# Kernel tuning notes

Hardware: AMD Instinct MI355X
Metric: run time of the kernel (lower is better)

The kernel has to match this reference:

```python
import math
import jax, jax.numpy as jnp
import numpy as np

D = 128
B = 8
PIXEL_SIZE = 1.5
GRID_DIST = 6.0
GRID_STEP = 3.0
TOP_K = 1
MAX_SHIFT_FRACTION = 0.25


def _euler_zyz_to_matrix(ang):
    # R = Z(a) @ Y(b) @ Z(c)  (pytorch3d 'ZYZ' convention, used by RELION)
    a, b, c = ang[..., 0], ang[..., 1], ang[..., 2]
    ca, sa = jnp.cos(a), jnp.sin(a)
    cb, sb = jnp.cos(b), jnp.sin(b)
    cc, sc = jnp.cos(c), jnp.sin(c)
    one = jnp.ones_like(a)
    r0 = jnp.stack([ca * cb * cc - sa * sc, -ca * cb * sc - sa * cc, ca * sb], -1)
    r1 = jnp.stack([sa * cb * cc + ca * sc, -sa * cb * sc + ca * cc, sa * sb], -1)
    r2 = jnp.stack([-sb * cc, sb * sc, cb * one], -1)
    return jnp.stack([r0, r1, r2], -2)


def _matrix_to_euler_zyz(R):
    b = jnp.arccos(jnp.clip(R[..., 2, 2], -1.0, 1.0))
    a = jnp.arctan2(R[..., 1, 2], R[..., 0, 2])
    c = jnp.arctan2(R[..., 2, 1], -R[..., 2, 0])
    return jnp.stack([a, b, c], -1)


def _so3_delta_grid():
    n = math.ceil(GRID_DIST * 2 / GRID_STEP)
    n = n if n % 2 == 1 else n + 1
    v = jnp.linspace(-GRID_DIST, GRID_DIST, n, dtype=jnp.float32)
    return jnp.stack(jnp.meshgrid(v, v, v, indexing='ij'), -1).reshape(-1, 3)


def _circular_mask(d):
    r = d // 2
    c = d // 2
    yy, xx = jnp.meshgrid(jnp.arange(d) - c, jnp.arange(d) - c, indexing='ij')
    return (yy * yy + xx * xx <= r * r).astype(jnp.float32)


def _fft_volume(vol):
    # fftshifted rfft of the (centered) volume, as in compute_dft
    d = jnp.fft.fftshift(vol, axes=(-3, -2, -1))
    d = jnp.fft.rfftn(d, axes=(-3, -2, -1))
    return jnp.fft.fftshift(d, axes=(-3, -2))


def _fft_images(imgs):
    d = jnp.fft.fftshift(imgs, axes=(-2, -1))
    d = jnp.fft.rfftn(d, axes=(-2, -1))
    return jnp.fft.fftshift(d, axes=(-2,))


def _trilinear_complex(vol, coords):
    # vol: (D, D, D//2+1) complex; coords: (..., 3) float zyx array indices.
    # Zero-padding outside the volume (grid_sample-like).
    shp = jnp.array(vol.shape, jnp.int32)
    c0f = jnp.floor(coords)
    frac = coords - c0f
    c0 = c0f.astype(jnp.int32)
    out = jnp.zeros(coords.shape[:-1], dtype=vol.dtype)
    for dz in (0, 1):
        for dy in (0, 1):
            for dx in (0, 1):
                sel = jnp.array([dz, dy, dx], bool)
                ci = c0 + jnp.array([dz, dy, dx], jnp.int32)
                w = jnp.where(sel, frac, 1.0 - frac).prod(-1)
                valid = jnp.all((ci >= 0) & (ci < shp), axis=-1)
                cc = jnp.clip(ci, 0, shp - 1)
                v = vol[cc[..., 0], cc[..., 1], cc[..., 2]]
                out = out + jnp.where(valid, w, 0.0) * v
    return out


def _extract_central_slices_rfft(vol_rfft, rotmats):
    # rotmats rotate xyz coords; volume dft is fftshifted along (-3,-2).
    d = vol_rfft.shape[0]
    fy = jnp.fft.fftshift(jnp.fft.fftfreq(d)).astype(jnp.float32)
    fx = jnp.fft.rfftfreq(d).astype(jnp.float32)
    gy, gx = jnp.meshgrid(fy, fx, indexing='ij')
    grid = jnp.stack([jnp.zeros_like(gy), gy, gx], -1)  # (d, d//2+1, 3) zyx, z=0 plane
    Rz = rotmats[..., ::-1, ::-1]  # xyz matrix -> acts on zyx coords
    coords = jnp.einsum('nij,hwj->nhwi', Rz, grid)  # (n, h, w, 3)
    conj_mask = coords[..., 2] < 0  # redundant half -> conjugate symmetry
    coords = jnp.where(conj_mask[..., None], -coords, coords)
    idx = jnp.stack([coords[..., 0] * d + d // 2,
                     coords[..., 1] * d + d // 2,
                     coords[..., 2] * d], -1)
    samples = _trilinear_complex(vol_rfft, idx)
    return jnp.where(conj_mask, jnp.conj(samples), samples)


def _forward(vol, imgs, ctfs, rotmats):
    d = vol.shape[-1]
    bsize = imgs.shape[0]
    imgs = imgs * _circular_mask(d)
    fparts = _fft_images(imgs)  # (B, d, d//2+1)
    vol_rfft = _fft_volume(vol)
    euler_degs = jnp.rad2deg(_matrix_to_euler_zyz(rotmats))  # (B, 3)
    delta = _so3_delta_grid()  # (O, 3)
    n_opts = delta.shape[0]
    expanded = delta[None] + euler_degs[:, None]  # (B, O, 3)
    rot = _euler_zyz_to_matrix(jnp.deg2rad(expanded.reshape(-1, 3)))
    projs = _extract_central_slices_rfft(vol_rfft, rot)
    projs = projs.reshape(bsize, n_opts, d, d // 2 + 1)
    projs = projs * ctfs[:, None].astype(projs.dtype)  # CTF multiply
    # FFT cross-correlation
    prod = fparts[:, None] * jnp.conj(projs)
    prod = jnp.fft.ifftshift(prod, axes=(-2,))
    corrs = jnp.fft.fftshift(jnp.fft.irfftn(prod, s=(d, d), axes=(-2, -1)), axes=(-2, -1))
    # constrained peak search within max_shift_fraction window around zero shift
    ctr = d // 2
    hw = int(MAX_SHIFT_FRACTION * d)
    win = corrs[..., ctr - hw:ctr + hw, ctr - hw:ctr + hw]
    flat = win.reshape(bsize, n_opts, -1)
    amax = jnp.argmax(flat, axis=-1)
    maxcorr = jnp.take_along_axis(flat, amax[..., None], -1)[..., 0]  # (B, O)
    row = amax // (2 * hw) + (ctr - hw)
    col = amax % (2 * hw) + (ctr - hw)
    shifts_xy = jnp.stack([col, row], -1)  # (B, O, 2) in full-image pixel coords
    # top-k over rotation candidates
    top_v, top_i = jax.lax.top_k(maxcorr, TOP_K)
    sel_shifts = jnp.take_along_axis(shifts_xy, top_i[..., None], axis=1)
    sel_euler = jnp.take_along_axis(expanded, top_i[..., None], axis=1)
    mean = maxcorr.mean(-1, keepdims=True)
    std = jnp.std(maxcorr, axis=-1, ddof=1, keepdims=True)
    weight = 0.5 * (1.0 + jax.lax.erf((top_v - mean) / ((std + 1e-6) * jnp.sqrt(jnp.float32(2.0)))))
    pred_shifts_angs = -(sel_shifts.astype(jnp.float32) - 0.5 * d) * PIXEL_SIZE
    pred_rotmats = _euler_zyz_to_matrix(jnp.deg2rad(sel_euler))
    return top_v, pred_rotmats, pred_shifts_angs, weight


def setup_inputs():
    key = jax.random.key(0)
    k1, k2, k3, k4 = jax.random.split(key, 4)
    vol = jax.random.normal(k1, (D, D, D), jnp.float32)
    imgs = jax.random.normal(k2, (B, D, D), jnp.float32)
    ctfs = jax.random.uniform(k3, (B, D, D // 2 + 1), jnp.float32, -1.0, 1.0)
    ang = jax.random.uniform(k4, (B, 3), jnp.float32, 0.2, 2.8)
    rotmats = _euler_zyz_to_matrix(ang)
    return {"vol": vol, "imgs": imgs, "ctfs": ctfs, "rotmats": rotmats}


def reference(vol, imgs, ctfs, rotmats):
    return _forward(vol, imgs, ctfs, rotmats)
```

## Files before the change

### kernel.cpp

```cpp
#include <hip/hip_runtime.h>
#include <hip/hip_fp16.h>
#include <math.h>

#define DIMN 128
#define KXN  65
#define NBATCH 8
#define NOPT 125

__device__ __forceinline__ void fft_twiddles(float sigma, int lane,
                                             float* twr, float* twi){
  const float W = 0.04908738521234052f;
  float s, c;
  sincosf(sigma * W * (float)lane, &s, &c);
  twr[0] = c; twi[0] = s;
#pragma unroll
  for (int st = 1; st <= 6; ++st){
    int off = 64 >> st;
    int m = (lane & (off - 1)) << st;
    sincosf(sigma * W * (float)m, &s, &c);
    bool hi = (lane & off) != 0;
    twr[st] = hi ? c : 1.f;
    twi[st] = hi ? s : 0.f;
  }
}

__device__ __forceinline__ void wave_fft128(float& Ar, float& Ai, float& Br, float& Bi,
                                            const float* twr, const float* twi, int lane){
  {
    float dr = Ar - Br, di = Ai - Bi;
    Ar += Br; Ai += Bi;
    float nr = dr*twr[0] - di*twi[0];
    Bi = dr*twi[0] + di*twr[0];
    Br = nr;
  }
#pragma unroll
  for (int s = 1; s <= 6; ++s){
    int off = 64 >> s;
    float sgn = (lane & off) ? -1.f : 1.f;
    float pr = __shfl_xor(Ar, off, 64);
    float pi = __shfl_xor(Ai, off, 64);
    float dr = fmaf(Ar, sgn, pr);
    float di = fmaf(Ai, sgn, pi);
    Ar = dr*twr[s] - di*twi[s];
    Ai = dr*twi[s] + di*twr[s];
    pr = __shfl_xor(Br, off, 64);
    pi = __shfl_xor(Bi, off, 64);
    dr = fmaf(Br, sgn, pr);
    di = fmaf(Bi, sgn, pi);
    Br = dr*twr[s] - di*twi[s];
    Bi = dr*twi[s] + di*twr[s];
  }
}

__device__ __forceinline__ int bitrev7(int lane){
  return (int)(__brev((unsigned)lane) >> 25);
}

__device__ __forceinline__ float2 h2f2(unsigned u){
  union { unsigned u; __half2 h; } cv; cv.u = u;
  return __half22float2(cv.h);
}
__device__ __forceinline__ unsigned f2h2(float re, float im){
  union { unsigned u; __half2 h; } cv;
  cv.h = __float22half2_rn(make_float2(re, im));
  return cv.u;
}

__global__ __launch_bounds__(256) void k_pre1(const float* __restrict__ vol,
                                              const float* __restrict__ imgs,
                                              const float* __restrict__ ctfs,
                                              const float* __restrict__ rotm,
                                              float2* __restrict__ A_T,
                                              float2* __restrict__ AI_T,
                                              float* __restrict__ cfT,
                                              float* __restrict__ mats){
  __shared__ float2 Zbuf[4][128];
  __shared__ float Xr[65][9];
  __shared__ float Xi[65][9];
  int bid = blockIdx.x;
  int t = threadIdx.x, lane = t & 63, w = t >> 6;

  if (bid < 2176){
    bool isimg = (bid >= 2048);
    const float* src = isimg ? imgs : vol;
    float2* dst = isimg ? AI_T : A_T;
    int l0 = (isimg ? (bid - 2048) : bid) * 8;
    int l1 = l0 + 2*w, l2 = l1 + 1;
    float m1a = 1.f, m1b = 1.f, m2a = 1.f, m2b = 1.f;
    if (isimg){
      int y1 = l1 & 127, y2 = y1 + 1;
      int dy1 = y1 - 64, dy2 = y2 - 64;
      int dxa = lane - 64, dxb = lane;
      m1a = (dy1*dy1 + dxa*dxa <= 4096) ? 1.f : 0.f;
      m1b = (dy1*dy1 + dxb*dxb <= 4096) ? 1.f : 0.f;
      m2a = (dy2*dy2 + dxa*dxa <= 4096) ? 1.f : 0.f;
      m2b = (dy2*dy2 + dxb*dxb <= 4096) ? 1.f : 0.f;
    }
    float twr[7], twi[7];
    fft_twiddles(-1.f, lane, twr, twi);
    float Ar = src[l1*DIMN + lane]*m1a,      Ai = src[l2*DIMN + lane]*m2a;
    float Br = src[l1*DIMN + lane + 64]*m1b, Bi = src[l2*DIMN + lane + 64]*m2b;
    wave_fft128(Ar, Ai, Br, Bi, twr, twi, lane);
    int e = bitrev7(lane);
    Zbuf[w][e]   = make_float2(Ar, Ai);
    Zbuf[w][e+1] = make_float2(Br, Bi);
    __syncthreads();
    {
      int k = lane, m = (128 - k) & 127;
      float2 zk = Zbuf[w][k], zm = Zbuf[w][m];
      float s = (k & 1) ? -0.5f : 0.5f;
      int ly1 = 2*w, ly2 = ly1 + 1;
      Xr[k][ly1] = s*(zk.x + zm.x);  Xi[k][ly1] = s*(zk.y - zm.y);
      Xr[k][ly2] = s*(zk.y + zm.y);  Xi[k][ly2] = s*(zm.x - zk.x);
      if (lane == 0){
        float2 z64 = Zbuf[w][64];
        Xr[64][ly1] = z64.x; Xi[64][ly1] = 0.f;
        Xr[64][ly2] = z64.y; Xi[64][ly2] = 0.f;
      }
    }
    __syncthreads();
    int slab = l0 >> 7, y0 = l0 & 127;
    int kk = t >> 2, yo = (t & 3) * 2;
    float4 v = make_float4(Xr[kk][yo], Xi[kk][yo], Xr[kk][yo+1], Xi[kk][yo+1]);
    *(float4*)(dst + (size_t)(slab*KXN + kk)*DIMN + y0 + yo) = v;
    if (t < 4){
      int yo2 = t*2;
      float4 v2 = make_float4(Xr[64][yo2], Xi[64][yo2], Xr[64][yo2+1], Xi[64][yo2+1]);
      *(float4*)(dst + (size_t)(slab*KXN + 64)*DIMN + y0 + yo2) = v2;
    }
  } else if (bid < 2436){
    int idx = (bid - 2176)*256 + t;
    int x = idx % 65; int by = idx / 65; int y = by & 127; int b = by >> 7;
    cfT[((size_t)b*KXN + x)*DIMN + y] = ctfs[idx];
  } else {
    int tid = (bid - 2436)*256 + t;
    if (tid < NBATCH*NOPT){
      int b = tid / NOPT, o = tid - b*NOPT;
      const float* R = rotm + b*9;
      float beta  = acosf(fminf(1.f, fmaxf(-1.f, R[8])));
      float alpha = atan2f(R[5], R[2]);
      float gamma = atan2f(R[7], -R[6]);
      const float DEG = 57.29577951308232f;
      float e0 = alpha*DEG + 3.0f*(float)(o/25      - 2);
      float e1 = beta *DEG + 3.0f*(float)((o/5) % 5 - 2);
      float e2 = gamma*DEG + 3.0f*(float)(o % 5     - 2);
      const float RAD = 0.017453292519943295f;
      float sa, ca, sb, cb, sc, cc;
      sincosf(e0*RAD, &sa, &ca);
      sincosf(e1*RAD, &sb, &cb);
      sincosf(e2*RAD, &sc, &cc);
      float* m = mats + tid*12;
      m[0] = sb*sc;
      m[1] = -sa*cb*sc + ca*cc;
      m[2] = -ca*cb*sc - sa*cc;
      m[3] = -sb*cc;
      m[4] = sa*cb*cc + ca*sc;
      m[5] = ca*cb*cc - sa*sc;
      m[6] = e0; m[7] = e1; m[8] = e2;
    }
  }
}

__global__ __launch_bounds__(512) void k_pre2(const float2* __restrict__ A_T,
                                              const float2* __restrict__ AI_T,
                                              float2* __restrict__ B_T,
                                              float2* __restrict__ fpT){
  __shared__ float As[64][9], Ai_[64][9], Bs[64][9], Bi_[64][9];
  int bid = blockIdx.x;
  int t = threadIdx.x, lane = t & 63, w = t >> 6;
  float twr[7], twi[7];
  fft_twiddles(-1.f, lane, twr, twi);

  if (bid < 1040){
    int k = bid >> 4, z0 = (bid & 15) * 8;
    int col = (z0 + w)*KXN + k;
    const float2* base = A_T + (size_t)col*DIMN;
    float2 A = base[lane], B = base[lane + 64];
    wave_fft128(A.x, A.y, B.x, B.y, twr, twi, lane);
    int p = bitrev7(lane) >> 1;
    As[p][w] = A.x; Ai_[p][w] = A.y; Bs[p][w] = B.x; Bi_[p][w] = B.y;
    __syncthreads();
    int q = t >> 2, zo = (t & 3) * 2;
    int p2 = (((q & 126) + 64) & 127) >> 1;
    float4 v;
    if (q & 1) v = make_float4(-Bs[p2][zo], -Bi_[p2][zo], -Bs[p2][zo+1], -Bi_[p2][zo+1]);
    else       v = make_float4( As[p2][zo],  Ai_[p2][zo],  As[p2][zo+1],  Ai_[p2][zo+1]);
    *(float4*)(B_T + (size_t)(q*KXN + k)*DIMN + z0 + zo) = v;
  } else {
    int c0 = (bid - 1040) * 8;
    int col = c0 + w;
    const float2* base = AI_T + (size_t)col*DIMN;
    float2 A = base[lane], B = base[lane + 64];
    wave_fft128(A.x, A.y, B.x, B.y, twr, twi, lane);
    int p = bitrev7(lane) >> 1;
    As[p][w] = A.x; Ai_[p][w] = A.y; Bs[p][w] = B.x; Bi_[p][w] = B.y;
    __syncthreads();
    int c = t >> 6, qo = (t & 63) * 2;
    int p2 = ((qo + 64) & 127) >> 1;
    float4 v = make_float4(As[p2][c], Ai_[p2][c], -Bs[p2][c], -Bi_[p2][c]);
    *(float4*)(fpT + (size_t)(c0 + c)*DIMN + qo) = v;
  }
}

__global__ __launch_bounds__(512) void k_fz(const float2* __restrict__ B_T,
                                            float2* __restrict__ volF){
  __shared__ float As[64][9], Ai_[64][9], Bs[64][9], Bi_[64][9];
  int bid = blockIdx.x;
  int j = bid / 9, grp = bid - j*9;
  int k0 = grp * 8;
  int vw = (grp == 8) ? 1 : 8;
  int t = threadIdx.x, lane = t & 63, w = t >> 6;
  if (w < vw){
    float twr[7], twi[7];
    fft_twiddles(-1.f, lane, twr, twi);
    int col = j*KXN + k0 + w;
    const float2* base = B_T + (size_t)col*DIMN;
    float2 A = base[lane], B = base[lane + 64];
    wave_fft128(A.x, A.y, B.x, B.y, twr, twi, lane);
    int p = bitrev7(lane) >> 1;
    As[p][w] = A.x; Ai_[p][w] = A.y; Bs[p][w] = B.x; Bi_[p][w] = B.y;
  }
  __syncthreads();
  int q = t >> 2, ko = (t & 3) * 2;
  int p2 = (((q & 126) + 64) & 127) >> 1;
  float2* obase = volF + (size_t)(q*DIMN + j)*KXN + k0;
  if (q & 1){
    if (ko < vw)     obase[ko]   = make_float2(-Bs[p2][ko],   -Bi_[p2][ko]);
    if (ko + 1 < vw) obase[ko+1] = make_float2(-Bs[p2][ko+1], -Bi_[p2][ko+1]);
  } else {
    if (ko < vw)     obase[ko]   = make_float2( As[p2][ko],    Ai_[p2][ko]);
    if (ko + 1 < vw) obase[ko+1] = make_float2( As[p2][ko+1],  Ai_[p2][ko+1]);
  }
}

__global__ __launch_bounds__(256) void k_fat(const float2* __restrict__ volF,
                                             unsigned* __restrict__ FATh){
  int idx = blockIdx.x*256 + threadIdx.x;
  int x = idx % 65; int zy = idx / 65; int y = zy & 127; int z = zy >> 7;
  int z1 = min(z+1,127), y1 = min(y+1,127), x1 = min(x+1,64);
  const size_t s00 = ((size_t)z *128 + y )*65;
  const size_t s01 = ((size_t)z *128 + y1)*65;
  const size_t s10 = ((size_t)z1*128 + y )*65;
  const size_t s11 = ((size_t)z1*128 + y1)*65;
  float2 a0 = volF[s00+x], a1 = volF[s00+x1];
  float2 b0 = volF[s01+x], b1 = volF[s01+x1];
  float2 c0 = volF[s10+x], c1 = volF[s10+x1];
  float2 d0 = volF[s11+x], d1 = volF[s11+x1];
  uint4* o = (uint4*)(FATh + ((size_t)idx << 3));
  o[0] = make_uint4(f2h2(a0.x,a0.y), f2h2(a1.x,a1.y), f2h2(b0.x,b0.y), f2h2(b1.x,b1.y));
  o[1] = make_uint4(f2h2(c0.x,c0.y), f2h2(c1.x,c1.y), f2h2(d0.x,d0.y), f2h2(d1.x,d1.y));
}

__device__ __forceinline__ float2 prod_elem(int h, int kx,
                                            float c1z, float c1y, float c1x,
                                            float c2z, float c2y, float c2x,
                                            const unsigned* __restrict__ FATh,
                                            const float2* __restrict__ fpc,
                                            const float*  __restrict__ cfc){
  float fyv = (float)(h - 64) * 0.0078125f;
  float fxv = (float)kx * 0.0078125f;
  float cz = fyv*c1z + fxv*c2z;
  float cy = fyv*c1y + fxv*c2y;
  float cx = fyv*c1x + fxv*c2x;
  bool cj = (cx < 0.f);
  if (cj){ cz = -cz; cy = -cy; cx = -cx; }
  float pz = cz*128.f + 64.f;
  float py = cy*128.f + 64.f;
  float px = cx*128.f;
  float fz = floorf(pz), fy = floorf(py), fx = floorf(px);
  int iz = (int)fz, iy = (int)fy, ix = (int)fx;
  float tz = pz - fz, ty = py - fy, tx = px - fx;
  float wz0 = ((unsigned)iz < 128u) ? 1.f - tz : ((iz == -1) ? tz : 0.f);
  float wz1 = ((unsigned)iz < 127u) ? tz : 0.f;
  float wy0 = ((unsigned)iy < 128u) ? 1.f - ty : ((iy == -1) ? ty : 0.f);
  float wy1 = ((unsigned)iy < 127u) ? ty : 0.f;
  float wx0 = ((unsigned)ix < 65u)  ? 1.f - tx : ((ix == -1) ? tx : 0.f);
  float wx1 = ((unsigned)ix < 64u)  ? tx : 0.f;
  int bz = min(max(iz, 0), 127), by = min(max(iy, 0), 127), bx = min(max(ix, 0), 64);
  const uint4* F = (const uint4*)(FATh + ((((size_t)bz*128 + by)*65 + bx) << 3));
  uint4 u0 = F[0], u1 = F[1];
  float2 v000 = h2f2(u0.x), v001 = h2f2(u0.y), v010 = h2f2(u0.z), v011 = h2f2(u0.w);
  float2 v100 = h2f2(u1.x), v101 = h2f2(u1.y), v110 = h2f2(u1.z), v111 = h2f2(u1.w);
  float w00 = wz0*wy0, w01 = wz0*wy1, w10 = wz1*wy0, w11 = wz1*wy1;
  float ar = w00*(wx0*v000.x + wx1*v001.x) + w01*(wx0*v010.x + wx1*v011.x)
           + w10*(wx0*v100.x + wx1*v101.x) + w11*(wx0*v110.x + wx1*v111.x);
  float ai = w00*(wx0*v000.y + wx1*v001.y) + w01*(wx0*v010.y + wx1*v011.y)
           + w10*(wx0*v100.y + wx1*v101.y) + w11*(wx0*v110.y + wx1*v111.y);
  if (cj) ai = -ai;
  float ct = cfc[h];
  float Pr = ar*ct, Pi = ai*ct;
  float2 f = fpc[h];
  return make_float2(f.x*Pr + f.y*Pi, f.y*Pr - f.x*Pi);
}

__global__ __launch_bounds__(512, 8) void k_main(const unsigned* __restrict__ FATh,
                                                 const float2* __restrict__ fpT,
                                                 const float* __restrict__ cfT,
                                                 const float* __restrict__ mats,
                                                 float* __restrict__ bestv,
                                                 int* __restrict__ besti){
  __shared__ float2 Q[64*65];
  __shared__ float rvw[8];
  __shared__ int   riw[8];

  int t = threadIdx.x, lane = t & 63, g = t >> 6;
  int blk = blockIdx.x;
  int b = blk & 7;
  int o = blk >> 3;

  float twr[7], twi[7];
  fft_twiddles(1.f, lane, twr, twi);

  const float* mp = mats + (size_t)(b*NOPT + o)*12;
  float c1z = mp[0], c1y = mp[1], c1x = mp[2];
  float c2z = mp[3], c2y = mp[4], c2x = mp[5];
  const float2* fp = fpT + (size_t)b*KXN*DIMN;
  const float*  cf = cfT + (size_t)b*KXN*DIMN;

  int e = bitrev7(lane);
  int slA = (e + 32) & 127;
  bool inwin = (slA < 64);
  const float NRM = 6.103515625e-05f;

#pragma unroll 1
  for (int ci = 0; ci < 8; ++ci){
    int kx = 8*ci + g;
    const float2* fpc = fp + (size_t)kx*DIMN;
    const float*  cfc = cf + (size_t)kx*DIMN;
    float2 A = prod_elem(lane,      kx, c1z,c1y,c1x, c2z,c2y,c2x, FATh, fpc, cfc);
    float2 B = prod_elem(lane + 64, kx, c1z,c1y,c1x, c2z,c2y,c2x, FATh, fpc, cfc);
    wave_fft128(A.x, A.y, B.x, B.y, twr, twi, lane);
    if (inwin){
      Q[slA*KXN + kx]     = make_float2( A.x*NRM,  A.y*NRM);
      Q[(slA+1)*KXN + kx] = make_float2(-B.x*NRM, -B.y*NRM);
    }
  }
  if (g == 0){
    const int kx = 64;
    const float2* fpc = fp + (size_t)kx*DIMN;
    const float*  cfc = cf + (size_t)kx*DIMN;
    float2 A = prod_elem(lane,      kx, c1z,c1y,c1x, c2z,c2y,c2x, FATh, fpc, cfc);
    float2 B = prod_elem(lane + 64, kx, c1z,c1y,c1x, c2z,c2y,c2x, FATh, fpc, cfc);
    wave_fft128(A.x, A.y, B.x, B.y, twr, twi, lane);
    if (inwin){
      Q[slA*KXN + kx]     = make_float2( A.x*NRM,  A.y*NRM);
      Q[(slA+1)*KXN + kx] = make_float2(-B.x*NRM, -B.y*NRM);
    }
  }
  __syncthreads();

  float bv = -INFINITY; int bi = 0;
  int ra = 64 - lane;
#pragma unroll 1
  for (int pi = 0; pi < 4; ++pi){
    int r1 = (4*g + pi) << 1;
    float2 a1 = Q[r1*KXN + lane];
    float2 a2 = Q[(r1+1)*KXN + lane];
    float2 b1 = Q[r1*KXN + ra];
    float2 b2 = Q[(r1+1)*KXN + ra];
    if (lane == 0){ a1.y = 0.f; a2.y = 0.f; b1.y = 0.f; b2.y = 0.f; }
    else { b1.y = -b1.y; b2.y = -b2.y; }
    float zAr = a1.x - a2.y, zAi = a1.y + a2.x;
    float zBr = b1.x - b2.y, zBi = b1.y + b2.x;
    wave_fft128(zAr, zAi, zBr, zBi, twr, twi, lane);
    if (inwin){
      int i0 = (r1 << 6) + slA;
      if (zAr > bv || (zAr == bv && i0      < bi)){ bv = zAr; bi = i0; }
      if (zAi > bv || (zAi == bv && i0+64   < bi)){ bv = zAi; bi = i0+64; }
      if (zBr > bv || (zBr == bv && i0+1    < bi)){ bv = zBr; bi = i0+1; }
      if (zBi > bv || (zBi == bv && i0+65   < bi)){ bv = zBi; bi = i0+65; }
    }
  }

#pragma unroll
  for (int off = 32; off > 0; off >>= 1){
    float v2 = __shfl_down(bv, off, 64);
    int   i2 = __shfl_down(bi, off, 64);
    if (v2 > bv || (v2 == bv && i2 < bi)){ bv = v2; bi = i2; }
  }
  if (lane == 0){ rvw[g] = bv; riw[g] = bi; }
  __syncthreads();
  if (t == 0){
    float fv = rvw[0]; int fi = riw[0];
#pragma unroll
    for (int wv = 1; wv < 8; ++wv){
      float v2 = rvw[wv]; int i2 = riw[wv];
      if (v2 > fv || (v2 == fv && i2 < fi)){ fv = v2; fi = i2; }
    }
    bestv[b*NOPT + o] = fv; besti[b*NOPT + o] = fi;
  }
}

__global__ __launch_bounds__(64) void k_out(const float* __restrict__ bestv,
                                            const int* __restrict__ besti,
                                            const float* __restrict__ mats,
                                            float* __restrict__ out){
  int b = blockIdx.x;
  if (threadIdx.x != 0) return;
  float bv = -INFINITY; int bo = 0;
  for (int o = 0; o < NOPT; ++o){
    float v = bestv[b*NOPT + o];
    if (v > bv){ bv = v; bo = o; }
  }
  float sum = 0.f;
  for (int o = 0; o < NOPT; ++o) sum += bestv[b*NOPT + o];
  float mean = sum * (1.0f/125.0f);
  float ss = 0.f;
  for (int o = 0; o < NOPT; ++o){
    float d = bestv[b*NOPT + o] - mean;
    ss += d*d;
  }
  float stdv = sqrtf(ss * (1.0f/124.0f));

  int wi = besti[b*NOPT + bo];
  int row = (wi >> 6) + 32;
  int col = (wi & 63) + 32;

  out[b] = bv;
  const float* mm = mats + (size_t)(b*NOPT + bo)*12;
  const float RAD = 0.017453292519943295f;
  float sa, ca, sb, cb, sc, cc;
  sincosf(mm[6]*RAD, &sa, &ca);
  sincosf(mm[7]*RAD, &sb, &cb);
  sincosf(mm[8]*RAD, &sc, &cc);
  float* R = out + 8 + b*9;
  R[0] = ca*cb*cc - sa*sc;  R[1] = -ca*cb*sc - sa*cc;  R[2] = ca*sb;
  R[3] = sa*cb*cc + ca*sc;  R[4] = -sa*cb*sc + ca*cc;  R[5] = sa*sb;
  R[6] = -sb*cc;            R[7] = sb*sc;              R[8] = cb;
  out[80 + b*2 + 0] = -((float)col - 64.f) * 1.5f;
  out[80 + b*2 + 1] = -((float)row - 64.f) * 1.5f;
  float z = (bv - mean) / ((stdv + 1e-6f) * 1.4142135623730951f);
  out[96 + b] = 0.5f*(1.f + erff(z));
}

extern "C" void kernel_launch(void* const* d_in, const int* in_sizes, int n_in,
                              void* d_out, int out_size, void* d_ws, size_t ws_size,
                              hipStream_t stream){
  (void)in_sizes; (void)n_in; (void)out_size; (void)ws_size;
  const float* vol  = (const float*)d_in[0];
  const float* imgs = (const float*)d_in[1];
  const float* ctfs = (const float*)d_in[2];
  const float* rotm = (const float*)d_in[3];
  float* out = (float*)d_out;

  unsigned* FATh = (unsigned*)d_ws;
  float2* bufA  = (float2*)(FATh + ((size_t)DIMN*DIMN*KXN*8));
  float2* bufB  = bufA + (size_t)DIMN*DIMN*KXN;
  float2* imgT  = bufB + (size_t)DIMN*DIMN*KXN;
  float2* fpT   = imgT + (size_t)NBATCH*KXN*DIMN;
  float*  cfT   = (float*)(fpT + (size_t)NBATCH*KXN*DIMN);
  float*  mats  = cfT + (size_t)NBATCH*KXN*DIMN;
  float*  bestv = mats + 12000;
  int*    besti = (int*)(bestv + 1000);

  k_pre1<<<2440, 256, 0, stream>>>(vol, imgs, ctfs, rotm, bufA, imgT, cfT, mats);
  k_pre2<<<1105, 512, 0, stream>>>(bufA, imgT, bufB, fpT);
  k_fz<<<1152, 512, 0, stream>>>(bufB, bufA);
  k_fat<<<(DIMN*DIMN*KXN)/256, 256, 0, stream>>>(bufA, FATh);
  k_main<<<NBATCH*NOPT, 512, 0, stream>>>(FATh, fpT, cfT, mats, bestv, besti);
  k_out<<<NBATCH, 64, 0, stream>>>(bestv, besti, mats, out);
}
```

Measured before the change: 114.8 us.

## Halve fat-voxel gather table to 4-neighbour fp16 records; parallelize final reduction

The precomputed trilinear table now stores only the four z/y neighbours per voxel (16 bytes) instead of all eight corners (32 bytes). The sampler fetches two adjacent records along x to rebuild the eight corners. This halves the table-build write traffic and the workspace footprint, at the cost of two separate 16-byte loads per sample, which may coalesce worse. The main loop is also unrolled by 2, and the per-batch output reduction switches from one serial thread to a wave-level shuffle reduction.

```diff
diff --git a/kernel.cpp b/kernel.cpp
--- a/kernel.cpp
+++ b/kernel.cpp
@@ -234,27 +234,21 @@
 }
 
 __global__ __launch_bounds__(256) void k_fat(const float2* __restrict__ volF,
-                                             unsigned* __restrict__ FATh){
+                                             uint4* __restrict__ FATy){
   int idx = blockIdx.x*256 + threadIdx.x;
   int x = idx % 65; int zy = idx / 65; int y = zy & 127; int z = zy >> 7;
-  int z1 = min(z+1,127), y1 = min(y+1,127), x1 = min(x+1,64);
-  const size_t s00 = ((size_t)z *128 + y )*65;
-  const size_t s01 = ((size_t)z *128 + y1)*65;
-  const size_t s10 = ((size_t)z1*128 + y )*65;
-  const size_t s11 = ((size_t)z1*128 + y1)*65;
-  float2 a0 = volF[s00+x], a1 = volF[s00+x1];
-  float2 b0 = volF[s01+x], b1 = volF[s01+x1];
-  float2 c0 = volF[s10+x], c1 = volF[s10+x1];
-  float2 d0 = volF[s11+x], d1 = volF[s11+x1];
-  uint4* o = (uint4*)(FATh + ((size_t)idx << 3));
-  o[0] = make_uint4(f2h2(a0.x,a0.y), f2h2(a1.x,a1.y), f2h2(b0.x,b0.y), f2h2(b1.x,b1.y));
-  o[1] = make_uint4(f2h2(c0.x,c0.y), f2h2(c1.x,c1.y), f2h2(d0.x,d0.y), f2h2(d1.x,d1.y));
+  int z1 = min(z+1,127), y1 = min(y+1,127);
+  float2 a = volF[((size_t)z *128 + y )*65 + x];
+  float2 b = volF[((size_t)z *128 + y1)*65 + x];
+  float2 c = volF[((size_t)z1*128 + y )*65 + x];
+  float2 d = volF[((size_t)z1*128 + y1)*65 + x];
+  FATy[idx] = make_uint4(f2h2(a.x,a.y), f2h2(b.x,b.y), f2h2(c.x,c.y), f2h2(d.x,d.y));
 }
 
 __device__ __forceinline__ float2 prod_elem(int h, int kx,
                                             float c1z, float c1y, float c1x,
                                             float c2z, float c2y, float c2x,
-                                            const unsigned* __restrict__ FATh,
+                                            const uint4* __restrict__ FATy,
                                             const float2* __restrict__ fpc,
                                             const float*  __restrict__ cfc){
   float fyv = (float)(h - 64) * 0.0078125f;
@@ -277,10 +271,11 @@
   float wx0 = ((unsigned)ix < 65u)  ? 1.f - tx : ((ix == -1) ? tx : 0.f);
   float wx1 = ((unsigned)ix < 64u)  ? tx : 0.f;
   int bz = min(max(iz, 0), 127), by = min(max(iy, 0), 127), bx = min(max(ix, 0), 64);
-  const uint4* F = (const uint4*)(FATh + ((((size_t)bz*128 + by)*65 + bx) << 3));
-  uint4 u0 = F[0], u1 = F[1];
-  float2 v000 = h2f2(u0.x), v001 = h2f2(u0.y), v010 = h2f2(u0.z), v011 = h2f2(u0.w);
-  float2 v100 = h2f2(u1.x), v101 = h2f2(u1.y), v110 = h2f2(u1.z), v111 = h2f2(u1.w);
+  int bx1 = min(bx + 1, 64);
+  const uint4* Fb = FATy + ((size_t)bz*128 + by)*65;
+  uint4 F0 = Fb[bx], F1 = Fb[bx1];
+  float2 v000 = h2f2(F0.x), v010 = h2f2(F0.y), v100 = h2f2(F0.z), v110 = h2f2(F0.w);
+  float2 v001 = h2f2(F1.x), v011 = h2f2(F1.y), v101 = h2f2(F1.z), v111 = h2f2(F1.w);
   float w00 = wz0*wy0, w01 = wz0*wy1, w10 = wz1*wy0, w11 = wz1*wy1;
   float ar = w00*(wx0*v000.x + wx1*v001.x) + w01*(wx0*v010.x + wx1*v011.x)
            + w10*(wx0*v100.x + wx1*v101.x) + w11*(wx0*v110.x + wx1*v111.x);
@@ -293,7 +288,7 @@
   return make_float2(f.x*Pr + f.y*Pi, f.y*Pr - f.x*Pi);
 }
 
-__global__ __launch_bounds__(512, 8) void k_main(const unsigned* __restrict__ FATh,
+__global__ __launch_bounds__(512, 8) void k_main(const uint4* __restrict__ FATy,
                                                  const float2* __restrict__ fpT,
                                                  const float* __restrict__ cfT,
                                                  const float* __restrict__ mats,
@@ -322,13 +317,13 @@
   bool inwin = (slA < 64);
   const float NRM = 6.103515625e-05f;
 
-#pragma unroll 1
+#pragma unroll 2
   for (int ci = 0; ci < 8; ++ci){
     int kx = 8*ci + g;
     const float2* fpc = fp + (size_t)kx*DIMN;
     const float*  cfc = cf + (size_t)kx*DIMN;
-    float2 A = prod_elem(lane,      kx, c1z,c1y,c1x, c2z,c2y,c2x, FATh, fpc, cfc);
-    float2 B = prod_elem(lane + 64, kx, c1z,c1y,c1x, c2z,c2y,c2x, FATh, fpc, cfc);
+    float2 A = prod_elem(lane,      kx, c1z,c1y,c1x, c2z,c2y,c2x, FATy, fpc, cfc);
+    float2 B = prod_elem(lane + 64, kx, c1z,c1y,c1x, c2z,c2y,c2x, FATy, fpc, cfc);
     wave_fft128(A.x, A.y, B.x, B.y, twr, twi, lane);
     if (inwin){
       Q[slA*KXN + kx]     = make_float2( A.x*NRM,  A.y*NRM);
@@ -339,8 +334,8 @@
     const int kx = 64;
     const float2* fpc = fp + (size_t)kx*DIMN;
     const float*  cfc = cf + (size_t)kx*DIMN;
-    float2 A = prod_elem(lane,      kx, c1z,c1y,c1x, c2z,c2y,c2x, FATh, fpc, cfc);
-    float2 B = prod_elem(lane + 64, kx, c1z,c1y,c1x, c2z,c2y,c2x, FATh, fpc, cfc);
+    float2 A = prod_elem(lane,      kx, c1z,c1y,c1x, c2z,c2y,c2x, FATy, fpc, cfc);
+    float2 B = prod_elem(lane + 64, kx, c1z,c1y,c1x, c2z,c2y,c2x, FATy, fpc, cfc);
     wave_fft128(A.x, A.y, B.x, B.y, twr, twi, lane);
     if (inwin){
       Q[slA*KXN + kx]     = make_float2( A.x*NRM,  A.y*NRM);
@@ -395,42 +390,53 @@
                                             const int* __restrict__ besti,
                                             const float* __restrict__ mats,
                                             float* __restrict__ out){
-  int b = blockIdx.x;
-  if (threadIdx.x != 0) return;
-  float bv = -INFINITY; int bo = 0;
-  for (int o = 0; o < NOPT; ++o){
-    float v = bestv[b*NOPT + o];
-    if (v > bv){ bv = v; bo = o; }
-  }
-  float sum = 0.f;
-  for (int o = 0; o < NOPT; ++o) sum += bestv[b*NOPT + o];
+  int b = blockIdx.x, lane = threadIdx.x;
+  const float* bvp = bestv + b*NOPT;
+  float v1 = (lane      < NOPT) ? bvp[lane]      : -INFINITY;
+  float v2 = (lane + 64 < NOPT) ? bvp[lane + 64] : -INFINITY;
+  float s1 = (lane      < NOPT) ? v1 : 0.f;
+  float s2 = (lane + 64 < NOPT) ? v2 : 0.f;
+  float bv; int bo;
+  if (v2 > v1){ bv = v2; bo = lane + 64; } else { bv = v1; bo = lane; }
+  float sum = s1 + s2;
+#pragma unroll
+  for (int off = 32; off > 0; off >>= 1){
+    float mv = __shfl_down(bv, off, 64);
+    int   mo = __shfl_down(bo, off, 64);
+    sum += __shfl_down(sum, off, 64);
+    if (mv > bv || (mv == bv && mo < bo)){ bv = mv; bo = mo; }
+  }
+  bv  = __shfl(bv, 0, 64);
+  bo  = __shfl(bo, 0, 64);
+  sum = __shfl(sum, 0, 64);
   float mean = sum * (1.0f/125.0f);
-  float ss = 0.f;
-  for (int o = 0; o < NOPT; ++o){
-    float d = bestv[b*NOPT + o] - mean;
-    ss += d*d;
-  }
-  float stdv = sqrtf(ss * (1.0f/124.0f));
-
-  int wi = besti[b*NOPT + bo];
-  int row = (wi >> 6) + 32;
-  int col = (wi & 63) + 32;
-
-  out[b] = bv;
-  const float* mm = mats + (size_t)(b*NOPT + bo)*12;
-  const float RAD = 0.017453292519943295f;
-  float sa, ca, sb, cb, sc, cc;
-  sincosf(mm[6]*RAD, &sa, &ca);
-  sincosf(mm[7]*RAD, &sb, &cb);
-  sincosf(mm[8]*RAD, &sc, &cc);
-  float* R = out + 8 + b*9;
-  R[0] = ca*cb*cc - sa*sc;  R[1] = -ca*cb*sc - sa*cc;  R[2] = ca*sb;
-  R[3] = sa*cb*cc + ca*sc;  R[4] = -sa*cb*sc + ca*cc;  R[5] = sa*sb;
-  R[6] = -sb*cc;            R[7] = sb*sc;              R[8] = cb;
-  out[80 + b*2 + 0] = -((float)col - 64.f) * 1.5f;
-  out[80 + b*2 + 1] = -((float)row - 64.f) * 1.5f;
-  float z = (bv - mean) / ((stdv + 1e-6f) * 1.4142135623730951f);
-  out[96 + b] = 0.5f*(1.f + erff(z));
+  float d1 = (lane      < NOPT) ? (v1 - mean) : 0.f;
+  float d2 = (lane + 64 < NOPT) ? (v2 - mean) : 0.f;
+  float ss = d1*d1 + d2*d2;
+#pragma unroll
+  for (int off = 32; off > 0; off >>= 1) ss += __shfl_down(ss, off, 64);
+
+  if (lane == 0){
+    float stdv = sqrtf(ss * (1.0f/124.0f));
+    int wi = besti[b*NOPT + bo];
+    int row = (wi >> 6) + 32;
+    int col = (wi & 63) + 32;
+    out[b] = bv;
+    const float* mm = mats + (size_t)(b*NOPT + bo)*12;
+    const float RAD = 0.017453292519943295f;
+    float sa, ca, sb, cb, sc, cc;
+    sincosf(mm[6]*RAD, &sa, &ca);
+    sincosf(mm[7]*RAD, &sb, &cb);
+    sincosf(mm[8]*RAD, &sc, &cc);
+    float* R = out + 8 + b*9;
+    R[0] = ca*cb*cc - sa*sc;  R[1] = -ca*cb*sc - sa*cc;  R[2] = ca*sb;
+    R[3] = sa*cb*cc + ca*sc;  R[4] = -sa*cb*sc + ca*cc;  R[5] = sa*sb;
+    R[6] = -sb*cc;            R[7] = sb*sc;              R[8] = cb;
+    out[80 + b*2 + 0] = -((float)col - 64.f) * 1.5f;
+    out[80 + b*2 + 1] = -((float)row - 64.f) * 1.5f;
+    float z = (bv - mean) / ((stdv + 1e-6f) * 1.4142135623730951f);
+    out[96 + b] = 0.5f*(1.f + erff(z));
+  }
 }
 
 extern "C" void kernel_launch(void* const* d_in, const int* in_sizes, int n_in,
@@ -443,8 +449,8 @@
   const float* rotm = (const float*)d_in[3];
   float* out = (float*)d_out;
 
-  unsigned* FATh = (unsigned*)d_ws;
-  float2* bufA  = (float2*)(FATh + ((size_t)DIMN*DIMN*KXN*8));
+  uint4* FATy  = (uint4*)d_ws;
+  float2* bufA  = (float2*)(FATy + (size_t)DIMN*DIMN*KXN);
   float2* bufB  = bufA + (size_t)DIMN*DIMN*KXN;
   float2* imgT  = bufB + (size_t)DIMN*DIMN*KXN;
   float2* fpT   = imgT + (size_t)NBATCH*KXN*DIMN;
@@ -456,7 +462,7 @@
   k_pre1<<<2440, 256, 0, stream>>>(vol, imgs, ctfs, rotm, bufA, imgT, cfT, mats);
   k_pre2<<<1105, 512, 0, stream>>>(bufA, imgT, bufB, fpT);
   k_fz<<<1152, 512, 0, stream>>>(bufB, bufA);
-  k_fat<<<(DIMN*DIMN*KXN)/256, 256, 0, stream>>>(bufA, FATh);
-  k_main<<<NBATCH*NOPT, 512, 0, stream>>>(FATh, fpT, cfT, mats, bestv, besti);
+  k_fat<<<(DIMN*DIMN*KXN)/256, 256, 0, stream>>>(bufA, FATy);
+  k_main<<<NBATCH*NOPT, 512, 0, stream>>>(FATy, fpT, cfT, mats, bestv, besti);
   k_out<<<NBATCH, 64, 0, stream>>>(bestv, besti, mats, out);
 }
```

After: 116.8 us. Within noise of the previous version (+1.7%).
